# Performance work log

Hardware: AMD Instinct MI355X
Metric: run time of the kernel (lower is better)

Reference implementation:

```python
import jax, jax.numpy as jnp
import numpy as np

V_PATCH = (1, 2, 4, 8, 16, 32)
RESI = 0.5   # abs(quant_resi)
BETA = 0.25
K_PHI = 4    # share_quant_resi


def _phi_idx(si, SN, K=K_PHI):
    # PhiPartiallyShared.__getitem__ with at = si/(SN-1)
    ticks = np.linspace(1/3/K, 1 - 1/3/K, K) if K == 4 else np.linspace(1/2/K, 1 - 1/2/K, K)
    return int(np.argmin(np.abs(ticks - si / (SN - 1))))


def _area_down(x, pn):
    # F.interpolate mode='area' with pn | H  == exact block mean
    B, C, H, W = x.shape
    return x.reshape(B, C, pn, H // pn, pn, W // pn).mean(axis=(3, 5))


def _bilinear(x, size):
    # matches torch bilinear, align_corners=False, antialias=False (half-pixel centers)
    B, C, _, _ = x.shape
    return jax.image.resize(x, (B, C, size, size), method='bilinear', antialias=False)


def _down(x, pn, si):
    if pn == x.shape[2]:
        return x
    return _area_down(x, pn) if si <= 3 else _bilinear(x, pn)


def _phi_ada(h, w, b, fw, fb, sn):
    # Phi_ada: conv weight modulated by fc(SN); fc is zero-init but kept in the graph
    C = h.shape[1]
    cond = (fw[:, 0] * jnp.float32(sn) + fb).reshape(C, C, 1, 1)
    wmod = w * (1.0 + cond)
    y = jax.lax.conv_general_dilated(h, wmod, (1, 1), 'SAME',
                                     dimension_numbers=('NCHW', 'OIHW', 'NCHW'))
    y = y + b[None, :, None, None]
    return h * (1.0 - RESI) + y * RESI


def _forward(f, embed_w, conv_w, conv_b, fc_w, fc_b):
    B, C, H, W = f.shape
    SN = len(V_PATCH)
    f_ng = jax.lax.stop_gradient(f)
    f_rest = f_ng
    f_hat = jnp.zeros_like(f_ng)
    e_ng = jax.lax.stop_gradient(embed_w)            # embedding.weight.data
    e_sq = jnp.sum(e_ng * e_ng, axis=1)              # [V]
    vq_losses = []
    commit = jnp.float32(0.0)
    for si, pn in enumerate(V_PATCH):
        rest = f_rest if si == SN - 1 else _down(f_rest, pn, si)
        rest_NC = rest.transpose(0, 2, 3, 1).reshape(-1, C)          # [N,C]
        # squared L2 distances to codebook, argmin (non-differentiable)
        d = (jnp.sum(rest_NC * rest_NC, axis=1, keepdims=True)
             + e_sq - 2.0 * (rest_NC @ e_ng.T))                       # [N,V]
        idx = jnp.argmin(d, axis=1)                                   # [N]
        h = embed_w[idx].reshape(B, pn, pn, C).transpose(0, 3, 1, 2)  # [B,C,pn,pn]
        if si != SN - 1:
            h = _bilinear(h, H)
        k = _phi_idx(si, SN)
        h = _phi_ada(h, conv_w[k], conv_b[k], fc_w[k], fc_b[k], SN)
        f_hat = f_hat + h
        f_rest = f_rest - jax.lax.stop_gradient(h)    # grad through f_rest is killed by argmin anyway
        vq_losses.append(jnp.mean((f_hat - f_ng) ** 2))
        fh_ng = jax.lax.stop_gradient(f_hat)
        commit = commit + jnp.mean((_down(fh_ng, pn, si) - _down(f, pn, si)) ** 2) * BETA
    commit = commit / SN
    # straight-through estimator
    f_hat_out = jax.lax.stop_gradient(f_hat) - f_ng + f
    return f_hat_out, jnp.stack(vq_losses), commit


def setup_inputs() -> dict:
    key = jax.random.key(0)
    k1, k2, k3 = jax.random.split(key, 3)
    B, C, H, W = 32, 64, 32, 32
    V = 4096
    f_BChw = jax.random.normal(k1, (B, C, H, W), dtype=jnp.float32)
    embed_w = jax.random.normal(k2, (V, C), dtype=jnp.float32) * 0.5  # trunc_normal std=0.5
    conv_w = jax.random.normal(k3, (K_PHI, C, C, 3, 3), dtype=jnp.float32) * 0.02
    conv_b = jnp.zeros((K_PHI, C), dtype=jnp.float32)
    fc_w = jnp.zeros((K_PHI, C * C, 1), dtype=jnp.float32)  # Phi_ada.fc zero-init
    fc_b = jnp.zeros((K_PHI, C * C), dtype=jnp.float32)
    return {'f_BChw': f_BChw, 'embed_w': embed_w, 'conv_w': conv_w,
            'conv_b': conv_b, 'fc_w': fc_w, 'fc_b': fc_b}


def reference(f_BChw, embed_w, conv_w, conv_b, fc_w, fc_b):
    return _forward(f_BChw, embed_w, conv_w, conv_b, fc_w, fc_b)
```

## Files before the change

### kernel.cpp

```cpp
#include <hip/hip_runtime.h>
#include <cfloat>

#define N_ELEM 2097152
#define TAU 2.0e-2f

typedef short s16x8 __attribute__((ext_vector_type(8)));
typedef float f32x4 __attribute__((ext_vector_type(4)));

__device__ __forceinline__ unsigned short f2bf(float v) {
    unsigned u = __float_as_uint(v);
    u += 0x7FFFu + ((u >> 16) & 1u);
    return (unsigned short)(u >> 16);
}
__device__ __forceinline__ float bf2f(unsigned short h) {
    return __uint_as_float(((unsigned)h) << 16);
}

__device__ __forceinline__ float blockReduceSum(float v) {
    __shared__ float red[8];
    #pragma unroll
    for (int off = 32; off; off >>= 1) v += __shfl_down(v, off, 64);
    int wid = threadIdx.x >> 6, lane = threadIdx.x & 63;
    if (lane == 0) red[wid] = v;
    __syncthreads();
    float r = 0.f;
    if (threadIdx.x == 0) {
        int nw = ((int)blockDim.x + 63) >> 6;
        for (int w = 0; w < nw; ++w) r += red[w];
    }
    __syncthreads();
    return r;
}

__global__ void k_embprep(const float* __restrict__ e, float* __restrict__ hesq,
                          unsigned short* __restrict__ ehiN, unsigned short* __restrict__ eloN,
                          int* __restrict__ count) {
    if (blockIdx.x == 0 && threadIdx.x < 6) count[threadIdx.x] = 0;
    int v = blockIdx.x * 256 + threadIdx.x;
    if (v >= 4096) return;
    const float4* r = (const float4*)(e + (size_t)v * 64);
    float s = 0.f;
    #pragma unroll
    for (int i = 0; i < 16; ++i) {
        float4 a = r[i];
        s += a.x * a.x + a.y * a.y + a.z * a.z + a.w * a.w;
    }
    hesq[v] = 0.5f * s;
    for (int i = 0; i < 64; ++i) {
        float x = e[(size_t)v * 64 + i];
        unsigned short h = f2bf(x);
        ehiN[(size_t)v * 64 + i] = h ^ 0x8000u;
        eloN[(size_t)v * 64 + i] = f2bf(x - bf2f(h)) ^ 0x8000u;
    }
}

__global__ void k_wmod(const float* __restrict__ w, const float* __restrict__ fcw,
                       const float* __restrict__ fcb,
                       unsigned short* __restrict__ wh, unsigned short* __restrict__ wl) {
    int i = blockIdx.x * 256 + threadIdx.x;
    if (i >= 4 * 64 * 64 * 9) return;
    int k = i / (64 * 64 * 9);
    int r = i % (64 * 64 * 9);
    int oi = r / 9;
    int t = r % 9;
    int co = oi >> 6, ci = oi & 63;
    float cond = fcw[k * 4096 + oi] * 6.0f + fcb[k * 4096 + oi];
    float v = w[i] * (1.0f + cond);
    size_t o = ((size_t)(k * 9 + t) * 64 + co) * 64 + ci;
    unsigned short h = f2bf(v);
    wh[o] = h;
    wl[o] = f2bf(v - bf2f(h));
}

__global__ __launch_bounds__(256) void k_down_plane(
        const float* __restrict__ f, const float* __restrict__ fhat,
        float* __restrict__ restnc, unsigned short* __restrict__ dhi,
        unsigned short* __restrict__ dlo, float* __restrict__ cmpPrev, int pn) {
    __shared__ float hs[32][16];
    __shared__ float cr[32][16];
    __shared__ float pm[256];
    int bc = blockIdx.x;
    int c = bc & 63, b = bc >> 6;
    int t = threadIdx.x;
    const float4* fp = (const float4*)(f + (size_t)bc * 1024);
    const float4* hp = (const float4*)(fhat + (size_t)bc * 1024);
    float4 a = fp[t], q = hp[t];
    int r = t >> 3, c4 = t & 7;
    hs[r][c4 * 2]     = (a.x - q.x) + (a.y - q.y);
    hs[r][c4 * 2 + 1] = (a.z - q.z) + (a.w - q.w);
    __syncthreads();
    int cpp = 16 / pn;
    for (int i = t; i < 32 * pn; i += 256) {
        int rr = i / pn, px = i % pn;
        float s = 0.f;
        for (int j = 0; j < cpp; ++j) s += hs[rr][px * cpp + j];
        cr[rr][px] = s;
    }
    __syncthreads();
    int s_ = 32 / pn;
    float inv = 1.0f / (float)(s_ * s_);
    for (int p = t; p < pn * pn; p += 256) {
        int py = p / pn, px = p % pn;
        float s = 0.f;
        for (int j = 0; j < s_; ++j) s += cr[py * s_ + j][px];
        float m = s * inv;
        pm[p] = m;
        int n = (b * pn + py) * pn + px;
        size_t o = (size_t)n * 64 + c;
        unsigned short h = f2bf(m);
        restnc[o] = m;
        dhi[o] = h;
        dlo[o] = f2bf(m - bf2f(h));
    }
    if (pn >= 2) {
        __syncthreads();
        int pnp = pn >> 1;
        float m2 = 0.f;
        for (int p = t; p < pnp * pnp; p += 256) {
            int py = p / pnp, px = p % pnp;
            float mm = 0.25f * (pm[(2 * py) * pn + 2 * px] + pm[(2 * py) * pn + 2 * px + 1]
                              + pm[(2 * py + 1) * pn + 2 * px] + pm[(2 * py + 1) * pn + 2 * px + 1]);
            m2 += mm * mm;
        }
        m2 = blockReduceSum(m2);
        if (t == 0) cmpPrev[blockIdx.x] = m2;
    }
}

__global__ void k_trans_nc(const float* __restrict__ A, const float* __restrict__ Bt,
                           float* __restrict__ dst,
                           unsigned short* __restrict__ dhi, unsigned short* __restrict__ dlo,
                           float* __restrict__ cmp) {
    __shared__ float t[64][65];
    int b = blockIdx.x;
    int p0 = blockIdx.y * 64;
    int lane = threadIdx.x & 63, r4 = threadIdx.x >> 6;
    #pragma unroll
    for (int i = 0; i < 16; ++i) {
        int c = i * 4 + r4;
        size_t g = ((size_t)b * 64 + c) * 1024 + p0 + lane;
        t[c][lane] = A[g] - Bt[g];
    }
    __syncthreads();
    #pragma unroll
    for (int i = 0; i < 16; ++i) {
        int p = i * 4 + r4;
        size_t o = ((size_t)(b * 1024 + p0 + p)) * 64 + lane;
        float v = t[lane][p];
        unsigned short h = f2bf(v);
        dst[o] = v;
        dhi[o] = h;
        dlo[o] = f2bf(v - bf2f(h));
    }
    float m2s = 0.f;
    for (int i = threadIdx.x; i < 1024; i += 256) {
        int c = i & 63, px = i >> 6;
        float m = 0.25f * (t[c][2 * px] + t[c][2 * px + 1] + t[c][32 + 2 * px] + t[c][33 + 2 * px]);
        m2s += m * m;
    }
    m2s = blockReduceSum(m2s);
    if (threadIdx.x == 0) cmp[blockIdx.x * 16 + blockIdx.y] = m2s;
}

__global__ __launch_bounds__(256) void k_vq_mfma(
        const unsigned short* __restrict__ resthi, const unsigned short* __restrict__ restlo,
        const unsigned short* __restrict__ embhiN, const unsigned short* __restrict__ embloN,
        const float* __restrict__ hesq,
        float* __restrict__ m1v_, int* __restrict__ m1i_, float* __restrict__ m2v_,
        int N, int CPS) {
    __shared__ __align__(16) unsigned short lah[64 * 64];
    __shared__ __align__(16) unsigned short lal[64 * 64];
    __shared__ __align__(16) float lq[64];
    int tid = threadIdx.x;
    int lane = tid & 63, wv = tid >> 6;
    int split = blockIdx.y;
    int p0 = blockIdx.x * 128 + wv * 32;
    int cr = lane & 15, oct = lane >> 4;
    int ko8 = oct * 8;
    int ptA = p0 + cr, ptB = p0 + 16 + cr;
    int pA = min(ptA, N - 1), pB = min(ptB, N - 1);

    const unsigned short* ra = resthi + (size_t)pA * 64;
    const unsigned short* la = restlo + (size_t)pA * 64;
    const unsigned short* rb = resthi + (size_t)pB * 64;
    const unsigned short* lb = restlo + (size_t)pB * 64;
    s16x8 bhA0 = *(const s16x8*)(ra + ko8);
    s16x8 bhA1 = *(const s16x8*)(ra + 32 + ko8);
    s16x8 blA0 = *(const s16x8*)(la + ko8);
    s16x8 blA1 = *(const s16x8*)(la + 32 + ko8);
    s16x8 bhB0 = *(const s16x8*)(rb + ko8);
    s16x8 bhB1 = *(const s16x8*)(rb + 32 + ko8);
    s16x8 blB0 = *(const s16x8*)(lb + ko8);
    s16x8 blB1 = *(const s16x8*)(lb + 32 + ko8);

    float m1vA = FLT_MAX, m2vA = FLT_MAX; int m1iA = 0;
    float m1vB = FLT_MAX, m2vB = FLT_MAX; int m1iB = 0;
    int sw = (cr & 7) << 4;

    int cbeg = split * CPS;
    for (int oc = 0; oc < CPS; oc += 64) {
        int cb = cbeg + oc;
        __syncthreads();
        for (int t = tid; t < 512; t += 256) {
            int cc = t >> 3, part = t & 7;
            int bo = (cc * 128 + part * 16) ^ ((cc & 7) << 4);
            *(uint4*)((char*)lah + bo) = *(const uint4*)(embhiN + (size_t)(cb + cc) * 64 + part * 8);
            *(uint4*)((char*)lal + bo) = *(const uint4*)(embloN + (size_t)(cb + cc) * 64 + part * 8);
        }
        if (tid < 64) lq[tid] = hesq[cb + tid];
        __syncthreads();
        #pragma unroll
        for (int sub = 0; sub < 4; ++sub) {
            int rowb = (sub * 16 + cr) * 128;
            s16x8 ah0 = *(const s16x8*)((const char*)lah + ((rowb + ko8 * 2) ^ sw));
            s16x8 ah1 = *(const s16x8*)((const char*)lah + ((rowb + 64 + ko8 * 2) ^ sw));
            s16x8 al0 = *(const s16x8*)((const char*)lal + ((rowb + ko8 * 2) ^ sw));
            s16x8 al1 = *(const s16x8*)((const char*)lal + ((rowb + 64 + ko8 * 2) ^ sw));
            f32x4 q = *(const f32x4*)(lq + sub * 16 + oct * 4);
            int crow = cb + sub * 16 + oct * 4;
            f32x4 acc = q;
            acc = __builtin_amdgcn_mfma_f32_16x16x32_bf16(ah0, bhA0, acc, 0, 0, 0);
            acc = __builtin_amdgcn_mfma_f32_16x16x32_bf16(ah1, bhA1, acc, 0, 0, 0);
            acc = __builtin_amdgcn_mfma_f32_16x16x32_bf16(ah0, blA0, acc, 0, 0, 0);
            acc = __builtin_amdgcn_mfma_f32_16x16x32_bf16(ah1, blA1, acc, 0, 0, 0);
            acc = __builtin_amdgcn_mfma_f32_16x16x32_bf16(al0, bhA0, acc, 0, 0, 0);
            acc = __builtin_amdgcn_mfma_f32_16x16x32_bf16(al1, bhA1, acc, 0, 0, 0);
            #pragma unroll
            for (int r = 0; r < 4; ++r) {
                float s = acc[r];
                bool lt = s < m1vA;
                m2vA = fminf(fmaxf(s, m1vA), m2vA);
                m1iA = lt ? (crow + r) : m1iA;
                m1vA = fminf(s, m1vA);
            }
            f32x4 accB = q;
            accB = __builtin_amdgcn_mfma_f32_16x16x32_bf16(ah0, bhB0, accB, 0, 0, 0);
            accB = __builtin_amdgcn_mfma_f32_16x16x32_bf16(ah1, bhB1, accB, 0, 0, 0);
            accB = __builtin_amdgcn_mfma_f32_16x16x32_bf16(ah0, blB0, accB, 0, 0, 0);
            accB = __builtin_amdgcn_mfma_f32_16x16x32_bf16(ah1, blB1, accB, 0, 0, 0);
            accB = __builtin_amdgcn_mfma_f32_16x16x32_bf16(al0, bhB0, accB, 0, 0, 0);
            accB = __builtin_amdgcn_mfma_f32_16x16x32_bf16(al1, bhB1, accB, 0, 0, 0);
            #pragma unroll
            for (int r = 0; r < 4; ++r) {
                float s = accB[r];
                bool lt = s < m1vB;
                m2vB = fminf(fmaxf(s, m1vB), m2vB);
                m1iB = lt ? (crow + r) : m1iB;
                m1vB = fminf(s, m1vB);
            }
        }
    }
    #pragma unroll
    for (int off = 16; off <= 32; off <<= 1) {
        float o1 = __shfl_xor(m1vA, off, 64); int oi = __shfl_xor(m1iA, off, 64);
        float o2 = __shfl_xor(m2vA, off, 64);
        bool lt = o1 < m1vA;
        m2vA = fminf(fmaxf(o1, m1vA), fminf(m2vA, o2));
        m1vA = fminf(o1, m1vA);
        m1iA = lt ? oi : m1iA;
        o1 = __shfl_xor(m1vB, off, 64); oi = __shfl_xor(m1iB, off, 64);
        o2 = __shfl_xor(m2vB, off, 64);
        lt = o1 < m1vB;
        m2vB = fminf(fmaxf(o1, m1vB), fminf(m2vB, o2));
        m1vB = fminf(o1, m1vB);
        m1iB = lt ? oi : m1iB;
    }
    if (oct == 0) {
        if (ptA < N) { size_t o = (size_t)split * N + ptA; m1v_[o] = m1vA; m1i_[o] = m1iA; m2v_[o] = m2vA; }
        if (ptB < N) { size_t o = (size_t)split * N + ptB; m1v_[o] = m1vB; m1i_[o] = m1iB; m2v_[o] = m2vB; }
    }
}

__global__ void k_vq_combine(const float* __restrict__ m1v_, const int* __restrict__ m1i_,
                             const float* __restrict__ m2v_,
                             int* __restrict__ idx, int* __restrict__ flag, int* __restrict__ count,
                             unsigned long long* __restrict__ pmin, int N, int SPLITS) {
    int n = blockIdx.x * 256 + threadIdx.x;
    if (n >= N) return;
    float a1v = m1v_[n], a2v = m2v_[n];
    int a1i = m1i_[n];
    for (int s = 1; s < SPLITS; ++s) {
        size_t o = (size_t)s * N + n;
        float b1v = m1v_[o], b2v = m2v_[o];
        int b1i = m1i_[o];
        bool lt = b1v < a1v;
        a2v = fminf(fmaxf(b1v, a1v), fminf(a2v, b2v));
        a1v = fminf(b1v, a1v);
        a1i = lt ? b1i : a1i;
    }
    idx[n] = a1i;
    pmin[n] = 0xFFFFFFFFFFFFFFFFull;
    if (a2v - a1v < TAU) {
        int p = atomicAdd(count, 1);
        flag[p] = n;
    }
}

__global__ __launch_bounds__(256) void k_vq_exact(
        const float* __restrict__ restnc, const float* __restrict__ embed,
        const float* __restrict__ hesq, const int* __restrict__ flag,
        const int* __restrict__ count, unsigned long long* __restrict__ pmin) {
    __shared__ float rs[32 * 64];
    int tid = threadIdx.x;
    int lane = tid & 63;
    int cnt = *count;
    int nb = (cnt + 31) >> 5;
    int ntask = nb * 16;
    for (int task = blockIdx.x; task < ntask; task += gridDim.x) {
        int batch = task >> 4, spl = task & 15;
        int lbase = batch << 5;
        int npts = min(32, cnt - lbase);
        __syncthreads();
        for (int i = tid; i < npts * 64; i += 256) {
            int li = i >> 6;
            rs[i] = restnc[(size_t)flag[lbase + li] * 64 + (i & 63)];
        }
        __syncthreads();
        int code = spl * 256 + tid;
        const float4* e4 = (const float4*)(embed + (size_t)code * 64);
        float4 e[16];
        #pragma unroll
        for (int i = 0; i < 16; ++i) e[i] = e4[i];
        float hq = hesq[code];
        for (int p = 0; p < npts; ++p) {
            const float4* r4 = (const float4*)(rs + p * 64);
            float d0 = 0.f, d1 = 0.f, d2 = 0.f, d3 = 0.f;
            #pragma unroll
            for (int i = 0; i < 16; i += 4) {
                float4 e0 = e[i], e1 = e[i + 1], e2 = e[i + 2], e3 = e[i + 3];
                d0 += e0.x * r4[i].x     + e0.y * r4[i].y     + e0.z * r4[i].z     + e0.w * r4[i].w;
                d1 += e1.x * r4[i + 1].x + e1.y * r4[i + 1].y + e1.z * r4[i + 1].z + e1.w * r4[i + 1].w;
                d2 += e2.x * r4[i + 2].x + e2.y * r4[i + 2].y + e2.z * r4[i + 2].z + e2.w * r4[i + 2].w;
                d3 += e3.x * r4[i + 3].x + e3.y * r4[i + 3].y + e3.z * r4[i + 3].z + e3.w * r4[i + 3].w;
            }
            float s = hq - ((d0 + d1) + (d2 + d3));
            unsigned u = __float_as_uint(s);
            u = (u & 0x80000000u) ? ~u : (u | 0x80000000u);
            unsigned long long pk = (((unsigned long long)u) << 32) | (unsigned)code;
            #pragma unroll
            for (int off = 32; off; off >>= 1) {
                unsigned long long o = __shfl_down(pk, off, 64);
                if (o < pk) pk = o;
            }
            if (lane == 0) atomicMin(pmin + flag[lbase + p], pk);
        }
    }
}

__global__ __launch_bounds__(512) void k_conv_mfma(
        const int* __restrict__ idx, const unsigned long long* __restrict__ pmin,
        const float* __restrict__ embed,
        const unsigned short* __restrict__ wh, const unsigned short* __restrict__ wl,
        const float* __restrict__ bias, const float* __restrict__ f_in,
        float* __restrict__ f_hat, float* __restrict__ vq_part, int pn) {
    __shared__ __align__(16) unsigned short Xh[6 * 34 * 64];
    __shared__ __align__(16) unsigned short Xl[6 * 34 * 64];
    __shared__ int pid[204][4];
    __shared__ float pwt[204][2];
    int b = blockIdx.x, rg = blockIdx.y;
    int y0 = rg * 4;
    int tid = threadIdx.x;
    int lane = tid & 63, wv = tid >> 6;
    int coh = (wv & 1) * 32;
    int ph  = (wv >> 1) * 2;
    int cr = lane & 15, oct = lane >> 4;

    if (tid < 204) {
        int lr = tid / 34, lc = tid % 34;
        int gy = y0 + lr - 1, gx = lc - 1;
        if (gy >= 0 && gy < 32 && gx >= 0 && gx < 32) {
            if (pn == 32) {
                int n = (b * 32 + gy) * 32 + gx;
                unsigned long long pv = pmin[n];
                int id = (pv != 0xFFFFFFFFFFFFFFFFull) ? (int)(pv & 0xFFFFFFFFull) : idx[n];
                pid[tid][0] = id;
            } else {
                float scale = (float)pn * (1.0f / 32.0f);
                float sy = (gy + 0.5f) * scale - 0.5f;
                float sx = (gx + 0.5f) * scale - 0.5f;
                float fy0 = floorf(sy), fx0 = floorf(sx);
                float wy = sy - fy0, wx = sx - fx0;
                int yy0 = max(0, min(pn - 1, (int)fy0));
                int yy1 = max(0, min(pn - 1, (int)fy0 + 1));
                int xx0 = max(0, min(pn - 1, (int)fx0));
                int xx1 = max(0, min(pn - 1, (int)fx0 + 1));
                int nb_ = b * pn * pn;
                int n00 = nb_ + yy0 * pn + xx0, n01 = nb_ + yy0 * pn + xx1;
                int n10 = nb_ + yy1 * pn + xx0, n11 = nb_ + yy1 * pn + xx1;
                unsigned long long p00 = pmin[n00], p01 = pmin[n01];
                unsigned long long p10 = pmin[n10], p11 = pmin[n11];
                pid[tid][0] = (p00 != 0xFFFFFFFFFFFFFFFFull) ? (int)(p00 & 0xFFFFFFFFull) : idx[n00];
                pid[tid][1] = (p01 != 0xFFFFFFFFFFFFFFFFull) ? (int)(p01 & 0xFFFFFFFFull) : idx[n01];
                pid[tid][2] = (p10 != 0xFFFFFFFFFFFFFFFFull) ? (int)(p10 & 0xFFFFFFFFull) : idx[n10];
                pid[tid][3] = (p11 != 0xFFFFFFFFFFFFFFFFull) ? (int)(p11 & 0xFFFFFFFFull) : idx[n11];
                pwt[tid][0] = wy; pwt[tid][1] = wx;
            }
        } else {
            pid[tid][0] = -1;
        }
    }
    __syncthreads();

    for (int q = tid; q < 204 * 8; q += 512) {
        int pl = q >> 3, o8 = q & 7;
        int lc = pl % 34;
        int bo = (pl * 128 + o8 * 16) ^ ((lc & 7) << 4);
        uint4 vh = {0, 0, 0, 0}, vl = {0, 0, 0, 0};
        int i00 = pid[pl][0];
        if (i00 >= 0) {
            union { unsigned short u[8]; uint4 v; } oh, ol;
            if (pn == 32) {
                const float4* e00 = (const float4*)(embed + (size_t)i00 * 64 + o8 * 8);
                #pragma unroll
                for (int half = 0; half < 2; ++half) {
                    float4 a00 = e00[half];
                    float vv[4] = {a00.x, a00.y, a00.z, a00.w};
                    #pragma unroll
                    for (int j = 0; j < 4; ++j) {
                        unsigned short h = f2bf(vv[j]);
                        oh.u[half * 4 + j] = h;
                        ol.u[half * 4 + j] = f2bf(vv[j] - bf2f(h));
                    }
                }
            } else {
                int i01 = pid[pl][1], i10 = pid[pl][2], i11 = pid[pl][3];
                float wy = pwt[pl][0], wx = pwt[pl][1];
                const float4* e00 = (const float4*)(embed + (size_t)i00 * 64 + o8 * 8);
                const float4* e01 = (const float4*)(embed + (size_t)i01 * 64 + o8 * 8);
                const float4* e10 = (const float4*)(embed + (size_t)i10 * 64 + o8 * 8);
                const float4* e11 = (const float4*)(embed + (size_t)i11 * 64 + o8 * 8);
                #pragma unroll
                for (int half = 0; half < 2; ++half) {
                    float4 a00 = e00[half], a01 = e01[half], a10 = e10[half], a11 = e11[half];
                    float t0, t1, vv[4];
                    t0 = a00.x + wx * (a01.x - a00.x); t1 = a10.x + wx * (a11.x - a10.x); vv[0] = t0 + wy * (t1 - t0);
                    t0 = a00.y + wx * (a01.y - a00.y); t1 = a10.y + wx * (a11.y - a10.y); vv[1] = t0 + wy * (t1 - t0);
                    t0 = a00.z + wx * (a01.z - a00.z); t1 = a10.z + wx * (a11.z - a10.z); vv[2] = t0 + wy * (t1 - t0);
                    t0 = a00.w + wx * (a01.w - a00.w); t1 = a10.w + wx * (a11.w - a10.w); vv[3] = t0 + wy * (t1 - t0);
                    #pragma unroll
                    for (int j = 0; j < 4; ++j) {
                        unsigned short h = f2bf(vv[j]);
                        oh.u[half * 4 + j] = h;
                        ol.u[half * 4 + j] = f2bf(vv[j] - bf2f(h));
                    }
                }
            }
            vh = oh.v; vl = ol.v;
        }
        *(uint4*)((char*)Xh + bo) = vh;
        *(uint4*)((char*)Xl + bo) = vl;
    }
    __syncthreads();

    f32x4 acc[2][2];
    #pragma unroll
    for (int ct = 0; ct < 2; ++ct)
        #pragma unroll
        for (int pp = 0; pp < 2; ++pp) acc[ct][pp] = (f32x4){0.f, 0.f, 0.f, 0.f};

    for (int t = 0; t < 9; ++t) {
        int dy = t / 3, dx = t % 3;
        #pragma unroll
        for (int cc = 0; cc < 2; ++cc) {
            size_t wo0 = ((size_t)t * 64 + coh + cr) * 64 + cc * 32 + oct * 8;
            size_t wo1 = ((size_t)t * 64 + coh + 16 + cr) * 64 + cc * 32 + oct * 8;
            s16x8 Ah0 = *(const s16x8*)(wh + wo0);
            s16x8 Al0 = *(const s16x8*)(wl + wo0);
            s16x8 Ah1 = *(const s16x8*)(wh + wo1);
            s16x8 Al1 = *(const s16x8*)(wl + wo1);
            #pragma unroll
            for (int pp = 0; pp < 2; ++pp) {
                int px = (ph + pp) * 16 + cr;
                int lr = (px >> 5) + dy;
                int lc = (px & 31) + dx;
                int bo = ((lr * 34 + lc) * 128 + cc * 64 + oct * 16) ^ ((lc & 7) << 4);
                s16x8 Bh = *(const s16x8*)((const char*)Xh + bo);
                s16x8 Bl = *(const s16x8*)((const char*)Xl + bo);
                acc[0][pp] = __builtin_amdgcn_mfma_f32_16x16x32_bf16(Ah0, Bh, acc[0][pp], 0, 0, 0);
                acc[0][pp] = __builtin_amdgcn_mfma_f32_16x16x32_bf16(Ah0, Bl, acc[0][pp], 0, 0, 0);
                acc[0][pp] = __builtin_amdgcn_mfma_f32_16x16x32_bf16(Al0, Bh, acc[0][pp], 0, 0, 0);
                acc[1][pp] = __builtin_amdgcn_mfma_f32_16x16x32_bf16(Ah1, Bh, acc[1][pp], 0, 0, 0);
                acc[1][pp] = __builtin_amdgcn_mfma_f32_16x16x32_bf16(Ah1, Bl, acc[1][pp], 0, 0, 0);
                acc[1][pp] = __builtin_amdgcn_mfma_f32_16x16x32_bf16(Al1, Bh, acc[1][pp], 0, 0, 0);
            }
        }
    }

    float local = 0.f;
    #pragma unroll
    for (int ct = 0; ct < 2; ++ct) {
        int cbase = coh + ct * 16 + oct * 4;
        #pragma unroll
        for (int pp = 0; pp < 2; ++pp) {
            int px = (ph + pp) * 16 + cr;
            int y = y0 + (px >> 5), x = px & 31;
            int lr = (px >> 5) + 1, lc = (px & 31) + 1;
            int bo = ((lr * 34 + lc) * 128 + cbase * 2) ^ ((lc & 7) << 4);
            ushort4 hvh = *(const ushort4*)((const char*)Xh + bo);
            ushort4 hvl = *(const ushort4*)((const char*)Xl + bo);
            #pragma unroll
            for (int r = 0; r < 4; ++r) {
                int co = cbase + r;
                unsigned short uh = (r == 0) ? hvh.x : (r == 1) ? hvh.y : (r == 2) ? hvh.z : hvh.w;
                unsigned short ul = (r == 0) ? hvl.x : (r == 1) ? hvl.y : (r == 2) ? hvl.z : hvl.w;
                float hv = bf2f(uh) + bf2f(ul);
                float hconv = acc[ct][pp][r] + bias[co];
                float hout = 0.5f * hv + 0.5f * hconv;
                size_t o = (((size_t)(b * 64 + co)) * 32 + y) * 32 + x;
                float fh = f_hat[o] + hout;
                f_hat[o] = fh;
                float d = fh - f_in[o];
                local += d * d;
            }
        }
    }
    local = blockReduceSum(local);
    if (tid == 0) vq_part[b * 8 + rg] = local;
}

__global__ void k_final(const float* __restrict__ vqp, const float* __restrict__ cmpP,
                        float* __restrict__ out) {
    const int pn2s[5] = {1, 4, 16, 64, 256};
    const int slots[5] = {2048, 2048, 2048, 2048, 512};
    __shared__ float commit_s;
    if (threadIdx.x == 0) commit_s = 0.f;
    __syncthreads();
    for (int si = 0; si < 6; ++si) {
        float l = vqp[si * 256 + threadIdx.x];
        l = blockReduceSum(l);
        if (threadIdx.x == 0) {
            float vl = l / (float)N_ELEM;
            out[N_ELEM + si] = vl;
            if (si == 5) commit_s += vl * 0.25f;
        }
        if (si < 5) {
            float csum = 0.f;
            for (int i = threadIdx.x; i < slots[si]; i += 256) csum += cmpP[si * 2048 + i];
            csum = blockReduceSum(csum);
            if (threadIdx.x == 0) commit_s += csum / (float)(2048 * pn2s[si]) * 0.25f;
        }
    }
    __syncthreads();
    if (threadIdx.x == 0) out[N_ELEM + 6] = commit_s / 6.0f;
}

extern "C" void kernel_launch(void* const* d_in, const int* in_sizes, int n_in,
                              void* d_out, int out_size, void* d_ws, size_t ws_size,
                              hipStream_t stream) {
    const float* f     = (const float*)d_in[0];
    const float* embed = (const float*)d_in[1];
    const float* convw = (const float*)d_in[2];
    const float* convb = (const float*)d_in[3];
    const float* fcw   = (const float*)d_in[4];
    const float* fcb   = (const float*)d_in[5];
    float* out = (float*)d_out;
    float* ws  = (float*)d_ws;

    float* restnc = ws + 2097152;
    unsigned short* resthi = (unsigned short*)(ws + 4194304);
    unsigned short* restlo = (unsigned short*)(ws + 5242880);
    unsigned short* embhiN = (unsigned short*)(ws + 6291456);
    unsigned short* embloN = (unsigned short*)(ws + 6422528);
    unsigned short* wmodh  = (unsigned short*)(ws + 6553600);
    unsigned short* wmodl  = (unsigned short*)(ws + 6627328);
    float* hesq   = ws + 6701056;
    float* m1v    = ws + 6705152;
    float* m2v    = ws + 6967296;
    int*   m1i    = (int*)(ws + 7229440);
    int*   idx    = (int*)(ws + 7491584);
    int*   flag   = (int*)(ws + 7524352);
    int*   count  = (int*)(ws + 7557120);
    unsigned long long* pmin = (unsigned long long*)(ws + 7557184);
    float* vqp    = ws + 7622720;
    float* cmpP   = ws + 7624256;

    hipMemsetAsync(d_out, 0, (size_t)out_size * sizeof(float), stream);
    k_wmod<<<576, 256, 0, stream>>>(convw, fcw, fcb, wmodh, wmodl);
    k_embprep<<<16, 256, 0, stream>>>(embed, hesq, embhiN, embloN, count);

    const int pns[6]    = {1, 2, 4, 8, 16, 32};
    const int splits[6] = {64, 64, 64, 64, 16, 8};
    const int kidx[6]   = {0, 0, 1, 2, 3, 3};

    for (int si = 0; si < 6; ++si) {
        int pn = pns[si], pn2 = pn * pn;
        int N = 32 * pn2, SPL = splits[si], CPS = 4096 / SPL;

        if (si <= 4) {
            k_down_plane<<<2048, 256, 0, stream>>>(f, out, restnc, resthi, restlo,
                                                   si >= 1 ? cmpP + (si - 1) * 2048 : nullptr, pn);
        } else {
            k_trans_nc<<<dim3(32, 16), 256, 0, stream>>>(f, out, restnc, resthi, restlo,
                                                         cmpP + 4 * 2048);
        }

        k_vq_mfma<<<dim3((N + 127) / 128, SPL), 256, 0, stream>>>(resthi, restlo, embhiN, embloN, hesq,
                                                                  m1v, m1i, m2v, N, CPS);
        k_vq_combine<<<(N + 255) / 256, 256, 0, stream>>>(m1v, m1i, m2v, idx, flag, count + si, pmin, N, SPL);
        k_vq_exact<<<512, 256, 0, stream>>>(restnc, embed, hesq, flag, count + si, pmin);

        k_conv_mfma<<<dim3(32, 8), 512, 0, stream>>>(idx, pmin, embed,
                                                     wmodh + kidx[si] * 36864, wmodl + kidx[si] * 36864,
                                                     convb + kidx[si] * 64, f, out, vqp + si * 256, pn);
    }

    k_final<<<1, 256, 0, stream>>>(vqp, cmpP, out);
}
```

Measured before the change: 587.1 us.

## Merge prep kernels, use fmed3 for second-min tracking, fold bias into accumulators

Merges the conv-weight modulation and codebook prep into one launch, saving a kernel launch. Replaces fmin/fmax pairs in the top-2 tracking with a single fmed3 instruction in the VQ inner loop and its reductions. Seeds the conv accumulators with the bias instead of adding it per element. Halves the codebook split count for the last scale, which gives fewer partial results to combine but less grid parallelism.

```diff
diff --git a/kernel.cpp b/kernel.cpp
--- a/kernel.cpp
+++ b/kernel.cpp
@@ -32,12 +32,29 @@
     return r;
 }
 
-__global__ void k_embprep(const float* __restrict__ e, float* __restrict__ hesq,
-                          unsigned short* __restrict__ ehiN, unsigned short* __restrict__ eloN,
-                          int* __restrict__ count) {
-    if (blockIdx.x == 0 && threadIdx.x < 6) count[threadIdx.x] = 0;
-    int v = blockIdx.x * 256 + threadIdx.x;
-    if (v >= 4096) return;
+__global__ void k_prep(const float* __restrict__ w, const float* __restrict__ fcw,
+                       const float* __restrict__ fcb,
+                       unsigned short* __restrict__ wh, unsigned short* __restrict__ wl,
+                       const float* __restrict__ e, float* __restrict__ hesq,
+                       unsigned short* __restrict__ ehiN, unsigned short* __restrict__ eloN,
+                       int* __restrict__ count) {
+    if (blockIdx.x < 576) {
+        int i = blockIdx.x * 256 + threadIdx.x;
+        int k = i / (64 * 64 * 9);
+        int r = i % (64 * 64 * 9);
+        int oi = r / 9;
+        int t = r % 9;
+        int co = oi >> 6, ci = oi & 63;
+        float cond = fcw[k * 4096 + oi] * 6.0f + fcb[k * 4096 + oi];
+        float v = w[i] * (1.0f + cond);
+        size_t o = ((size_t)(k * 9 + t) * 64 + co) * 64 + ci;
+        unsigned short h = f2bf(v);
+        wh[o] = h;
+        wl[o] = f2bf(v - bf2f(h));
+        return;
+    }
+    if (blockIdx.x == 576 && threadIdx.x < 6) count[threadIdx.x] = 0;
+    int v = (blockIdx.x - 576) * 256 + threadIdx.x;
     const float4* r = (const float4*)(e + (size_t)v * 64);
     float s = 0.f;
     #pragma unroll
@@ -52,24 +69,6 @@
         ehiN[(size_t)v * 64 + i] = h ^ 0x8000u;
         eloN[(size_t)v * 64 + i] = f2bf(x - bf2f(h)) ^ 0x8000u;
     }
-}
-
-__global__ void k_wmod(const float* __restrict__ w, const float* __restrict__ fcw,
-                       const float* __restrict__ fcb,
-                       unsigned short* __restrict__ wh, unsigned short* __restrict__ wl) {
-    int i = blockIdx.x * 256 + threadIdx.x;
-    if (i >= 4 * 64 * 64 * 9) return;
-    int k = i / (64 * 64 * 9);
-    int r = i % (64 * 64 * 9);
-    int oi = r / 9;
-    int t = r % 9;
-    int co = oi >> 6, ci = oi & 63;
-    float cond = fcw[k * 4096 + oi] * 6.0f + fcb[k * 4096 + oi];
-    float v = w[i] * (1.0f + cond);
-    size_t o = ((size_t)(k * 9 + t) * 64 + co) * 64 + ci;
-    unsigned short h = f2bf(v);
-    wh[o] = h;
-    wl[o] = f2bf(v - bf2f(h));
 }
 
 __global__ __launch_bounds__(256) void k_down_plane(
@@ -229,7 +228,7 @@
             for (int r = 0; r < 4; ++r) {
                 float s = acc[r];
                 bool lt = s < m1vA;
-                m2vA = fminf(fmaxf(s, m1vA), m2vA);
+                m2vA = __builtin_amdgcn_fmed3f(s, m1vA, m2vA);
                 m1iA = lt ? (crow + r) : m1iA;
                 m1vA = fminf(s, m1vA);
             }
@@ -244,7 +243,7 @@
             for (int r = 0; r < 4; ++r) {
                 float s = accB[r];
                 bool lt = s < m1vB;
-                m2vB = fminf(fmaxf(s, m1vB), m2vB);
+                m2vB = __builtin_amdgcn_fmed3f(s, m1vB, m2vB);
                 m1iB = lt ? (crow + r) : m1iB;
                 m1vB = fminf(s, m1vB);
             }
@@ -255,13 +254,13 @@
         float o1 = __shfl_xor(m1vA, off, 64); int oi = __shfl_xor(m1iA, off, 64);
         float o2 = __shfl_xor(m2vA, off, 64);
         bool lt = o1 < m1vA;
-        m2vA = fminf(fmaxf(o1, m1vA), fminf(m2vA, o2));
+        m2vA = fminf(__builtin_amdgcn_fmed3f(o1, m1vA, m2vA), o2);
         m1vA = fminf(o1, m1vA);
         m1iA = lt ? oi : m1iA;
         o1 = __shfl_xor(m1vB, off, 64); oi = __shfl_xor(m1iB, off, 64);
         o2 = __shfl_xor(m2vB, off, 64);
         lt = o1 < m1vB;
-        m2vB = fminf(fmaxf(o1, m1vB), fminf(m2vB, o2));
+        m2vB = fminf(__builtin_amdgcn_fmed3f(o1, m1vB, m2vB), o2);
         m1vB = fminf(o1, m1vB);
         m1iB = lt ? oi : m1iB;
     }
@@ -284,7 +283,7 @@
         float b1v = m1v_[o], b2v = m2v_[o];
         int b1i = m1i_[o];
         bool lt = b1v < a1v;
-        a2v = fminf(fmaxf(b1v, a1v), fminf(a2v, b2v));
+        a2v = fminf(__builtin_amdgcn_fmed3f(b1v, a1v, a2v), b2v);
         a1v = fminf(b1v, a1v);
         a1i = lt ? b1i : a1i;
     }
@@ -452,11 +451,11 @@
     }
     __syncthreads();
 
+    f32x4 b0 = *(const f32x4*)(bias + coh + oct * 4);
+    f32x4 b1 = *(const f32x4*)(bias + coh + 16 + oct * 4);
     f32x4 acc[2][2];
     #pragma unroll
-    for (int ct = 0; ct < 2; ++ct)
-        #pragma unroll
-        for (int pp = 0; pp < 2; ++pp) acc[ct][pp] = (f32x4){0.f, 0.f, 0.f, 0.f};
+    for (int pp = 0; pp < 2; ++pp) { acc[0][pp] = b0; acc[1][pp] = b1; }
 
     for (int t = 0; t < 9; ++t) {
         int dy = t / 3, dx = t % 3;
@@ -504,8 +503,7 @@
                 unsigned short uh = (r == 0) ? hvh.x : (r == 1) ? hvh.y : (r == 2) ? hvh.z : hvh.w;
                 unsigned short ul = (r == 0) ? hvl.x : (r == 1) ? hvl.y : (r == 2) ? hvl.z : hvl.w;
                 float hv = bf2f(uh) + bf2f(ul);
-                float hconv = acc[ct][pp][r] + bias[co];
-                float hout = 0.5f * hv + 0.5f * hconv;
+                float hout = 0.5f * hv + 0.5f * acc[ct][pp][r];
                 size_t o = (((size_t)(b * 64 + co)) * 32 + y) * 32 + x;
                 float fh = f_hat[o] + hout;
                 f_hat[o] = fh;
@@ -575,11 +573,11 @@
     float* cmpP   = ws + 7624256;
 
     hipMemsetAsync(d_out, 0, (size_t)out_size * sizeof(float), stream);
-    k_wmod<<<576, 256, 0, stream>>>(convw, fcw, fcb, wmodh, wmodl);
-    k_embprep<<<16, 256, 0, stream>>>(embed, hesq, embhiN, embloN, count);
+    k_prep<<<592, 256, 0, stream>>>(convw, fcw, fcb, wmodh, wmodl,
+                                    embed, hesq, embhiN, embloN, count);
 
     const int pns[6]    = {1, 2, 4, 8, 16, 32};
-    const int splits[6] = {64, 64, 64, 64, 16, 8};
+    const int splits[6] = {64, 64, 64, 64, 16, 4};
     const int kidx[6]   = {0, 0, 1, 2, 3, 3};
 
     for (int si = 0; si < 6; ++si) {
```

Result: no change. 583.5 us (-0.6%).
